# Performance work log

Hardware: AMD Instinct MI355X
Metric: run time of the kernel (lower is better)

Reference implementation:

```python
import jax, jax.numpy as jnp
import numpy as np

B, S, H = 256, 196, 1024  # batch, image_size**2, hidden_size


def _linear_init(key, fan_in, fan_out):
    kw, kb = jax.random.split(key)
    lim = 1.0 / np.sqrt(fan_in)
    W = jax.random.uniform(kw, (fan_in, fan_out), jnp.float32, -lim, lim)
    b = jax.random.uniform(kb, (fan_out,), jnp.float32, -lim, lim)
    return W, b


def setup_inputs() -> dict:
    key = jax.random.key(0)
    ks = jax.random.split(key, 7)
    v = jax.random.normal(ks[0], (B, S, H), jnp.float32)
    h = jax.random.normal(ks[1], (B, H), jnp.float32)
    W_fc, b_fc = _linear_init(ks[2], H, 2 * H)
    W_v, b_v = _linear_init(ks[3], H, H)
    W_h, b_h = _linear_init(ks[4], H, H)
    W_s, b_s = _linear_init(ks[5], H, H)
    W_z, b_z = _linear_init(ks[6], H, 1)
    return {"v": v, "h": h, "W_fc": W_fc, "b_fc": b_fc, "W_v": W_v, "b_v": b_v,
            "W_h": W_h, "b_h": b_h, "W_s": W_s, "b_s": b_s, "W_z": W_z, "b_z": b_z}


def reference(v, h, W_fc, b_fc, W_v, b_v, W_h, b_h, W_s, b_s, W_z, b_z):
    # Dropout is identity in eval mode.
    hs = jnp.tanh(h[:, None, :] @ W_fc + b_fc)          # (B, 1, 2H)
    h1, s = hs[..., :H], hs[..., H:]                    # each (B, 1, H)
    _v = v @ W_v + b_v                                  # (B, S, H)
    _h = h1 @ W_h + b_h                                 # (B, 1, H)
    _s = s @ W_s + b_s                                  # (B, 1, H)
    z = jnp.tanh(jnp.concatenate([_v, _s], axis=1) + _h)  # (B, S+1, H)
    z = (z @ W_z + b_z)[..., 0]                         # (B, S+1)
    a = jax.nn.softmax(z, axis=1)                       # (B, S+1)
    vc = jnp.concatenate([v, s], axis=1)                # (B, S+1, H)
    c = jnp.sum(a[:, :, None] * vc, axis=1)             # (B, H)
    return a, c
```

## Files before the change

### kernel.cpp

```cpp
#include <hip/hip_runtime.h>
#include <hip/hip_bf16.h>
#include <cstdint>
#include <cstddef>

#define Bb  256
#define Ss  196
#define Hh  1024
#define SP1 197
#define Mm  50176

typedef float  f32x4 __attribute__((ext_vector_type(4)));
typedef short  s16x8 __attribute__((ext_vector_type(8)));
typedef unsigned short u16;
typedef unsigned short u16x8 __attribute__((ext_vector_type(8)));

__device__ __forceinline__ u16 f2b(float f) {
  __hip_bfloat16 b = __float2bfloat16(f);
  u16 r; __builtin_memcpy(&r, &b, 2); return r;
}

__device__ __forceinline__ float ftanh(float x) {
  float ax = fabsf(x);
  float t = __expf(-2.f * ax);
  float r = (1.f - t) * __builtin_amdgcn_rcpf(1.f + t);
  return copysignf(r, x);
}

__global__ __launch_bounds__(256) void k_transpose_cvt(const float* __restrict__ Wv,
                                                       u16* __restrict__ WvT) {
  __shared__ float t[64][65];
  int k0 = (blockIdx.x & 15) * 64;
  int n0 = (blockIdx.x >> 4) * 64;
  int tid = threadIdx.x;
#pragma unroll
  for (int i = 0; i < 16; ++i) {
    int idx = i * 256 + tid;
    int r = idx >> 6, c = idx & 63;
    t[r][c] = Wv[(size_t)(k0 + r) * Hh + n0 + c];
  }
  __syncthreads();
#pragma unroll
  for (int i = 0; i < 16; ++i) {
    int idx = i * 256 + tid;
    int r = idx >> 6, c = idx & 63;
    WvT[(size_t)(n0 + r) * Hh + ((k0 + c) ^ ((r & 7) << 3))] = f2b(t[c][r]);
  }
}

__device__ __forceinline__ void small_gemm_core(int bid, int nct,
    const float* __restrict__ X, int ldx,
    const float* __restrict__ W, int ldw,
    const float* __restrict__ bias,
    float* __restrict__ Y, int ldy, int act) {
  __shared__ float xs[4][16][64];
  int tid = threadIdx.x, lane = tid & 63, w = tid >> 6;
  int ct = bid % nct, bt = bid / nct;
  int col = ct * 64 + lane;
  float acc[16];
#pragma unroll
  for (int b = 0; b < 16; ++b) acc[b] = 0.f;
  int xr = lane >> 2, xc = (lane & 3) * 16;
  for (int kc = 0; kc < 4; ++kc) {
    int kb = w * 256 + kc * 64;
#pragma unroll
    for (int q = 0; q < 4; ++q)
      *(f32x4*)&xs[w][xr][xc + q * 4] =
          *(const f32x4*)&X[(size_t)(bt * 16 + xr) * ldx + kb + xc + q * 4];
    for (int kl = 0; kl < 64; kl += 4) {
      float w0 = W[(size_t)(kb + kl + 0) * ldw + col];
      float w1 = W[(size_t)(kb + kl + 1) * ldw + col];
      float w2 = W[(size_t)(kb + kl + 2) * ldw + col];
      float w3 = W[(size_t)(kb + kl + 3) * ldw + col];
#pragma unroll
      for (int b = 0; b < 16; ++b) {
        f32x4 x = *(const f32x4*)&xs[w][b][kl];
        acc[b] += x.x * w0 + x.y * w1 + x.z * w2 + x.w * w3;
      }
    }
  }
#pragma unroll
  for (int b = 0; b < 16; ++b) xs[w][b][lane] = acc[b];
  __syncthreads();
#pragma unroll
  for (int q = 0; q < 4; ++q) {
    int b = w * 4 + q;
    float s = xs[0][b][lane] + xs[1][b][lane] + xs[2][b][lane] + xs[3][b][lane]
            + bias[col];
    if (act) s = ftanh(s);
    Y[(size_t)(bt * 16 + b) * ldy + col] = s;
  }
}

__global__ __launch_bounds__(256) void k_fc(const float* __restrict__ h,
                                            const float* __restrict__ Wfc,
                                            const float* __restrict__ bfc,
                                            float* __restrict__ hs) {
  small_gemm_core(blockIdx.x, 32, h, Hh, Wfc, 2048, bfc, hs, 2048, 1);
}

__global__ __launch_bounds__(256) void k_dual(const float* __restrict__ hs,
                                              const float* __restrict__ Wh,
                                              const float* __restrict__ bh,
                                              const float* __restrict__ Ws_,
                                              const float* __restrict__ bs_,
                                              float* __restrict__ hhp,
                                              float* __restrict__ svp) {
  int bid = blockIdx.x;
  int sel = bid >= 256;
  small_gemm_core(bid - (sel << 8), 16,
                  sel ? hs + 1024 : hs, 2048,
                  sel ? Ws_ : Wh, Hh,
                  sel ? bs_ : bh,
                  sel ? svp : hhp, Hh, 0);
}

#define BM 128
#define BN 256
#define BK 64
#define LDA 72
__global__ __launch_bounds__(256, 2) void k_big(const float* __restrict__ V,
                                                const u16* __restrict__ WvT,
                                                const float* __restrict__ bv,
                                                const float* __restrict__ hh,
                                                const float* __restrict__ Wz,
                                                float* __restrict__ zpart) {
  __shared__ __align__(16) u16 As[BM * LDA];
  __shared__ __align__(16) u16 Bs[BN * BK];
  __shared__ float wz_s[BN], bv_s[BN], hh_s[2][BN];
  __shared__ float zred[4][BM];

  int bid = blockIdx.x;
  int lin = (bid & 7) * 196 + (bid >> 3);
  int mt = lin >> 2, nt = lin & 3;
  int row0 = mt * BM, n0 = nt * BN;

  int tid = threadIdx.x;
  int lane = tid & 63, wid = tid >> 6;

  int b0 = row0 / Ss;
  int rsplit = (b0 + 1) * Ss - row0;
  int b1 = (rsplit < BM) ? b0 + 1 : b0;
  wz_s[tid] = Wz[n0 + tid];
  bv_s[tid] = bv[n0 + tid];
  hh_s[0][tid] = hh[(size_t)b0 * Hh + n0 + tid];
  hh_s[1][tid] = hh[(size_t)b1 * Hh + n0 + tid];

  f32x4 acc[8][4];
  f32x4 zz = {0.f, 0.f, 0.f, 0.f};
#pragma unroll
  for (int m = 0; m < 8; ++m)
#pragma unroll
    for (int n = 0; n < 4; ++n) acc[m][n] = zz;

  int arow = tid >> 3;
  int acol = (tid & 7) * 8;
  const float* Ap = V + (size_t)(row0 + arow) * Hh + acol;

  int bsub = lane >> 3;
  int bko  = (lane & 7) * 8;
  int bxor = (lane & 7) << 3;

  f32x4 av[8];
#pragma unroll
  for (int j = 0; j < 4; ++j) {
    av[2 * j]     = *(const f32x4*)(Ap + (size_t)j * 32 * Hh);
    av[2 * j + 1] = *(const f32x4*)(Ap + (size_t)j * 32 * Hh + 4);
  }

  for (int kt = 0; kt < 16; ++kt) {
    int k0 = kt * BK;
    __syncthreads();
#pragma unroll
    for (int i = 0; i < 8; ++i) {
      int r = wid * 64 + i * 8;
      const u16* g = WvT + (size_t)(n0 + r + bsub) * Hh + (k0 + bko);
      __builtin_amdgcn_global_load_lds(
          (const __attribute__((address_space(1))) unsigned int*)(const void*)g,
          (__attribute__((address_space(3))) unsigned int*)(void*)&Bs[r * BK],
          16, 0, 0);
    }
#pragma unroll
    for (int j = 0; j < 4; ++j) {
      u16x8 w;
      w[0] = f2b(av[2 * j].x);     w[1] = f2b(av[2 * j].y);
      w[2] = f2b(av[2 * j].z);     w[3] = f2b(av[2 * j].w);
      w[4] = f2b(av[2 * j + 1].x); w[5] = f2b(av[2 * j + 1].y);
      w[6] = f2b(av[2 * j + 1].z); w[7] = f2b(av[2 * j + 1].w);
      *(u16x8*)&As[(j * 32 + arow) * LDA + acol] = w;
    }
    if (kt < 15) {
#pragma unroll
      for (int j = 0; j < 4; ++j) {
        av[2 * j]     = *(const f32x4*)(Ap + (size_t)j * 32 * Hh + k0 + BK);
        av[2 * j + 1] = *(const f32x4*)(Ap + (size_t)j * 32 * Hh + k0 + BK + 4);
      }
    }
    __syncthreads();
#pragma unroll
    for (int ks = 0; ks < 2; ++ks) {
      int kk = ks * 32 + (lane >> 4) * 8;
      s16x8 afr[8], bfr[4];
#pragma unroll
      for (int m = 0; m < 8; ++m)
        afr[m] = *(const s16x8*)&As[(m * 16 + (lane & 15)) * LDA + kk];
#pragma unroll
      for (int n = 0; n < 4; ++n) {
        int r = wid * 64 + n * 16 + (lane & 15);
        bfr[n] = *(const s16x8*)&Bs[r * BK + (kk ^ bxor)];
      }
#pragma unroll
      for (int m = 0; m < 8; ++m)
#pragma unroll
        for (int n = 0; n < 4; ++n)
          acc[m][n] = __builtin_amdgcn_mfma_f32_16x16x32_bf16(afr[m], bfr[n], acc[m][n], 0, 0, 0);
    }
  }

  int cl = lane & 15, rg = lane >> 4;
  float pz[8][4];
#pragma unroll
  for (int m = 0; m < 8; ++m)
#pragma unroll
    for (int j = 0; j < 4; ++j) pz[m][j] = 0.f;
#pragma unroll
  for (int n = 0; n < 4; ++n) {
    int col = wid * 64 + n * 16 + cl;
    float wzv = wz_s[col], bvv = bv_s[col];
    float h0 = hh_s[0][col], h1 = hh_s[1][col];
#pragma unroll
    for (int m = 0; m < 8; ++m)
#pragma unroll
      for (int j = 0; j < 4; ++j) {
        int r = m * 16 + rg * 4 + j;
        float hv = (r >= rsplit) ? h1 : h0;
        pz[m][j] += wzv * ftanh(acc[m][n][j] + bvv + hv);
      }
  }
#pragma unroll
  for (int m = 0; m < 8; ++m)
#pragma unroll
    for (int j = 0; j < 4; ++j) {
      float vv = pz[m][j];
      vv += __shfl_xor(vv, 1); vv += __shfl_xor(vv, 2);
      vv += __shfl_xor(vv, 4); vv += __shfl_xor(vv, 8);
      pz[m][j] = vv;
    }
  if (cl == 0) {
#pragma unroll
    for (int m = 0; m < 8; ++m)
#pragma unroll
      for (int j = 0; j < 4; ++j)
        zred[wid][m * 16 + rg * 4 + j] = pz[m][j];
  }
  __syncthreads();
  if (tid < BM)
    zpart[(size_t)nt * Mm + row0 + tid] =
        zred[0][tid] + zred[1][tid] + zred[2][tid] + zred[3][tid];
}

__global__ __launch_bounds__(256) void k_softmax(const float* __restrict__ zpart,
                                                 const float* __restrict__ sv,
                                                 const float* __restrict__ hhp,
                                                 const float* __restrict__ Wz,
                                                 const float* __restrict__ bz,
                                                 float* __restrict__ outA) {
  int b = blockIdx.x, tid = threadIdx.x;
  int wid = tid >> 6, lane = tid & 63;
  __shared__ float redm[4], reds[4];
  __shared__ float zSsh;
  {
    int j0 = tid * 4;
    f32x4 s4 = *(const f32x4*)&sv[(size_t)b * Hh + j0];
    f32x4 h4 = *(const f32x4*)&hhp[(size_t)b * Hh + j0];
    f32x4 w4 = *(const f32x4*)&Wz[j0];
    float p = w4.x * ftanh(s4.x + h4.x) + w4.y * ftanh(s4.y + h4.y)
            + w4.z * ftanh(s4.z + h4.z) + w4.w * ftanh(s4.w + h4.w);
#pragma unroll
    for (int d = 1; d < 64; d <<= 1) p += __shfl_xor(p, d);
    if (lane == 0) redm[wid] = p;
    __syncthreads();
    if (tid == 0) zSsh = redm[0] + redm[1] + redm[2] + redm[3] + bz[0];
    __syncthreads();
  }
  float z = -1e30f;
  if (tid < Ss) {
    float s = 0.f;
#pragma unroll
    for (int nt = 0; nt < 4; ++nt) s += zpart[(size_t)nt * Mm + (size_t)b * Ss + tid];
    z = s + bz[0];
  } else if (tid == Ss) {
    z = zSsh;
  }
  float m = z;
#pragma unroll
  for (int d = 1; d < 64; d <<= 1) m = fmaxf(m, __shfl_xor(m, d));
  if (lane == 0) redm[wid] = m;
  __syncthreads();
  m = fmaxf(fmaxf(redm[0], redm[1]), fmaxf(redm[2], redm[3]));
  float e = (tid <= Ss) ? expf(z - m) : 0.f;
  float s = e;
#pragma unroll
  for (int d = 1; d < 64; d <<= 1) s += __shfl_xor(s, d);
  if (lane == 0) reds[wid] = s;
  __syncthreads();
  s = reds[0] + reds[1] + reds[2] + reds[3];
  if (tid <= Ss) outA[(size_t)b * SP1 + tid] = e / s;
}

__global__ __launch_bounds__(256) void k_ctx(const float* __restrict__ V,
                                             const float* __restrict__ hs,
                                             const float* __restrict__ A,
                                             float* __restrict__ outC) {
  int b = blockIdx.x >> 2;
  int col = (blockIdx.x & 3) * 256 + threadIdx.x;
  __shared__ float a_s[SP1];
  if (threadIdx.x < SP1) a_s[threadIdx.x] = A[(size_t)b * SP1 + threadIdx.x];
  __syncthreads();
  float acc = a_s[Ss] * hs[(size_t)b * 2048 + 1024 + col];
  const float* vb = &V[(size_t)b * Ss * Hh + col];
#pragma unroll 4
  for (int t = 0; t < Ss; ++t) acc += a_s[t] * vb[(size_t)t * Hh];
  outC[(size_t)b * Hh + col] = acc;
}

extern "C" void kernel_launch(void* const* d_in, const int* in_sizes, int n_in,
                              void* d_out, int out_size, void* d_ws, size_t ws_size,
                              hipStream_t stream) {
  const float* v   = (const float*)d_in[0];
  const float* h   = (const float*)d_in[1];
  const float* Wfc = (const float*)d_in[2];
  const float* bfc = (const float*)d_in[3];
  const float* Wv  = (const float*)d_in[4];
  const float* bv  = (const float*)d_in[5];
  const float* Wh  = (const float*)d_in[6];
  const float* bh  = (const float*)d_in[7];
  const float* Ws  = (const float*)d_in[8];
  const float* bs  = (const float*)d_in[9];
  const float* Wz  = (const float*)d_in[10];
  const float* bz  = (const float*)d_in[11];
  float* out  = (float*)d_out;
  float* outA = out;
  float* outC = out + (size_t)Bb * SP1;

  float* ws  = (float*)d_ws;
  float* hs  = ws;
  float* hh  = hs + 524288;
  float* sv  = hh + 262144;
  float* zp  = sv + 262144;
  u16*  WvT  = (u16*)(zp + 200704);

  k_transpose_cvt<<<256, 256, 0, stream>>>(Wv, WvT);
  k_fc<<<512, 256, 0, stream>>>(h, Wfc, bfc, hs);
  k_dual<<<512, 256, 0, stream>>>(hs, Wh, bh, Ws, bs, hh, sv);
  k_big<<<1568, 256, 0, stream>>>(v, WvT, bv, hh, Wz, zp);
  k_softmax<<<256, 256, 0, stream>>>(zp, sv, hh, Wz, bz, outA);
  k_ctx<<<1024, 256, 0, stream>>>(v, hs, outA, outC);
}
```

Before: 262.4 us.

## Pre-convert V to swizzled bf16, shrink GEMM tile, read bf16 V in context

Adds a pass that converts V to a swizzled bf16 copy in workspace. The main GEMM then streams A tiles straight to LDS through global_load_lds, and the tile shrinks from 128x256 to 128x128 on a 2x2 wave grid with higher occupancy. The context kernel reads the bf16 copy, halving its V traffic but applying bf16 rounding to V in the output c. The path only runs when the workspace is large enough, otherwise it falls back to fp32 V with the new tiling, and it adds an extra full read and write of V.

```diff
diff --git a/kernel.cpp b/kernel.cpp
--- a/kernel.cpp
+++ b/kernel.cpp
@@ -18,12 +18,19 @@
   __hip_bfloat16 b = __float2bfloat16(f);
   u16 r; __builtin_memcpy(&r, &b, 2); return r;
 }
-
+__device__ __forceinline__ float b2f(u16 u) {
+  return __uint_as_float(((unsigned)u) << 16);
+}
 __device__ __forceinline__ float ftanh(float x) {
   float ax = fabsf(x);
   float t = __expf(-2.f * ax);
   float r = (1.f - t) * __builtin_amdgcn_rcpf(1.f + t);
   return copysignf(r, x);
+}
+__device__ __forceinline__ void gload16(const u16* g, u16* l) {
+  __builtin_amdgcn_global_load_lds(
+      (const __attribute__((address_space(1))) unsigned int*)(const void*)g,
+      (__attribute__((address_space(3))) unsigned int*)(void*)l, 16, 0, 0);
 }
 
 __global__ __launch_bounds__(256) void k_transpose_cvt(const float* __restrict__ Wv,
@@ -45,6 +52,19 @@
     int r = idx >> 6, c = idx & 63;
     WvT[(size_t)(n0 + r) * Hh + ((k0 + c) ^ ((r & 7) << 3))] = f2b(t[c][r]);
   }
+}
+
+__global__ __launch_bounds__(256) void k_cvtV(const float* __restrict__ V,
+                                              u16* __restrict__ Vb) {
+  int c = blockIdx.x * 256 + threadIdx.x;
+  int m = c >> 7;
+  int k8 = (c & 127) << 3;
+  f32x4 a = *(const f32x4*)(V + (size_t)m * Hh + k8);
+  f32x4 b = *(const f32x4*)(V + (size_t)m * Hh + k8 + 4);
+  u16x8 w;
+  w[0] = f2b(a.x); w[1] = f2b(a.y); w[2] = f2b(a.z); w[3] = f2b(a.w);
+  w[4] = f2b(b.x); w[5] = f2b(b.y); w[6] = f2b(b.z); w[7] = f2b(b.w);
+  *(u16x8*)(Vb + (size_t)m * Hh + (k8 ^ ((m & 7) << 3))) = w;
 }
 
 __device__ __forceinline__ void small_gemm_core(int bid, int nct,
@@ -114,102 +134,108 @@
                   sel ? svp : hhp, Hh, 0);
 }
 
-#define BM 128
-#define BN 256
 #define BK 64
-#define LDA 72
-__global__ __launch_bounds__(256, 2) void k_big(const float* __restrict__ V,
-                                                const u16* __restrict__ WvT,
-                                                const float* __restrict__ bv,
-                                                const float* __restrict__ hh,
-                                                const float* __restrict__ Wz,
-                                                float* __restrict__ zpart) {
-  __shared__ __align__(16) u16 As[BM * LDA];
-  __shared__ __align__(16) u16 Bs[BN * BK];
-  __shared__ float wz_s[BN], bv_s[BN], hh_s[2][BN];
-  __shared__ float zred[4][BM];
+template<int PRE>
+__global__ __launch_bounds__(256, PRE ? 4 : 3)
+void k_big(const float* __restrict__ V, const u16* __restrict__ Vb,
+           const u16* __restrict__ WvT, const float* __restrict__ bv,
+           const float* __restrict__ hh, const float* __restrict__ Wz,
+           float* __restrict__ zpart) {
+  constexpr int LDA_ = PRE ? 64 : 72;
+  __shared__ __align__(16) u16 As[128 * LDA_];
+  __shared__ __align__(16) u16 Bs[128 * 64];
+  __shared__ float wz_s[128], bv_s[128], hh_s[2][128];
+  __shared__ float zred[4][64];
 
   int bid = blockIdx.x;
-  int lin = (bid & 7) * 196 + (bid >> 3);
-  int mt = lin >> 2, nt = lin & 3;
-  int row0 = mt * BM, n0 = nt * BN;
+  int lin = (bid & 7) * 392 + (bid >> 3);
+  int mt = lin >> 3, nt = lin & 7;
+  int row0 = mt * 128, n0 = nt * 128;
 
   int tid = threadIdx.x;
   int lane = tid & 63, wid = tid >> 6;
+  int wm = wid >> 1, wn = wid & 1;
 
   int b0 = row0 / Ss;
   int rsplit = (b0 + 1) * Ss - row0;
-  int b1 = (rsplit < BM) ? b0 + 1 : b0;
-  wz_s[tid] = Wz[n0 + tid];
-  bv_s[tid] = bv[n0 + tid];
-  hh_s[0][tid] = hh[(size_t)b0 * Hh + n0 + tid];
-  hh_s[1][tid] = hh[(size_t)b1 * Hh + n0 + tid];
-
-  f32x4 acc[8][4];
+  int b1 = (rsplit < 128) ? b0 + 1 : b0;
+  if (tid < 128) {
+    wz_s[tid] = Wz[n0 + tid];
+    bv_s[tid] = bv[n0 + tid];
+    hh_s[0][tid] = hh[(size_t)b0 * Hh + n0 + tid];
+    hh_s[1][tid] = hh[(size_t)b1 * Hh + n0 + tid];
+  }
+
+  f32x4 acc[4][4];
   f32x4 zz = {0.f, 0.f, 0.f, 0.f};
 #pragma unroll
-  for (int m = 0; m < 8; ++m)
+  for (int m = 0; m < 4; ++m)
 #pragma unroll
     for (int n = 0; n < 4; ++n) acc[m][n] = zz;
 
-  int arow = tid >> 3;
-  int acol = (tid & 7) * 8;
-  const float* Ap = V + (size_t)(row0 + arow) * Hh + acol;
-
-  int bsub = lane >> 3;
-  int bko  = (lane & 7) * 8;
+  int srow = lane >> 3, scol = (lane & 7) * 8;
   int bxor = (lane & 7) << 3;
 
+  int arow = tid >> 3, acol8 = (tid & 7) * 8;
+  const float* Ap = V + (size_t)(row0 + arow) * Hh + acol8;
   f32x4 av[8];
-#pragma unroll
-  for (int j = 0; j < 4; ++j) {
-    av[2 * j]     = *(const f32x4*)(Ap + (size_t)j * 32 * Hh);
-    av[2 * j + 1] = *(const f32x4*)(Ap + (size_t)j * 32 * Hh + 4);
+  if constexpr (!PRE) {
+#pragma unroll
+    for (int j = 0; j < 4; ++j) {
+      av[2 * j]     = *(const f32x4*)(Ap + (size_t)j * 32 * Hh);
+      av[2 * j + 1] = *(const f32x4*)(Ap + (size_t)j * 32 * Hh + 4);
+    }
   }
 
   for (int kt = 0; kt < 16; ++kt) {
     int k0 = kt * BK;
     __syncthreads();
 #pragma unroll
-    for (int i = 0; i < 8; ++i) {
-      int r = wid * 64 + i * 8;
-      const u16* g = WvT + (size_t)(n0 + r + bsub) * Hh + (k0 + bko);
-      __builtin_amdgcn_global_load_lds(
-          (const __attribute__((address_space(1))) unsigned int*)(const void*)g,
-          (__attribute__((address_space(3))) unsigned int*)(void*)&Bs[r * BK],
-          16, 0, 0);
-    }
-#pragma unroll
-    for (int j = 0; j < 4; ++j) {
-      u16x8 w;
-      w[0] = f2b(av[2 * j].x);     w[1] = f2b(av[2 * j].y);
-      w[2] = f2b(av[2 * j].z);     w[3] = f2b(av[2 * j].w);
-      w[4] = f2b(av[2 * j + 1].x); w[5] = f2b(av[2 * j + 1].y);
-      w[6] = f2b(av[2 * j + 1].z); w[7] = f2b(av[2 * j + 1].w);
-      *(u16x8*)&As[(j * 32 + arow) * LDA + acol] = w;
-    }
-    if (kt < 15) {
+    for (int i = 0; i < 4; ++i) {
+      int r = wid * 32 + i * 8;
+      gload16(WvT + (size_t)(n0 + r + srow) * Hh + k0 + scol, &Bs[r * 64]);
+    }
+    if constexpr (PRE) {
+#pragma unroll
+      for (int i = 0; i < 4; ++i) {
+        int r = wid * 32 + i * 8;
+        gload16(Vb + (size_t)(row0 + r + srow) * Hh + k0 + scol, &As[r * 64]);
+      }
+    } else {
 #pragma unroll
       for (int j = 0; j < 4; ++j) {
-        av[2 * j]     = *(const f32x4*)(Ap + (size_t)j * 32 * Hh + k0 + BK);
-        av[2 * j + 1] = *(const f32x4*)(Ap + (size_t)j * 32 * Hh + k0 + BK + 4);
+        u16x8 w;
+        w[0] = f2b(av[2 * j].x);     w[1] = f2b(av[2 * j].y);
+        w[2] = f2b(av[2 * j].z);     w[3] = f2b(av[2 * j].w);
+        w[4] = f2b(av[2 * j + 1].x); w[5] = f2b(av[2 * j + 1].y);
+        w[6] = f2b(av[2 * j + 1].z); w[7] = f2b(av[2 * j + 1].w);
+        *(u16x8*)&As[(j * 32 + arow) * LDA_ + acol8] = w;
+      }
+      if (kt < 15) {
+#pragma unroll
+        for (int j = 0; j < 4; ++j) {
+          av[2 * j]     = *(const f32x4*)(Ap + (size_t)j * 32 * Hh + k0 + BK);
+          av[2 * j + 1] = *(const f32x4*)(Ap + (size_t)j * 32 * Hh + k0 + BK + 4);
+        }
       }
     }
     __syncthreads();
 #pragma unroll
     for (int ks = 0; ks < 2; ++ks) {
       int kk = ks * 32 + (lane >> 4) * 8;
-      s16x8 afr[8], bfr[4];
-#pragma unroll
-      for (int m = 0; m < 8; ++m)
-        afr[m] = *(const s16x8*)&As[(m * 16 + (lane & 15)) * LDA + kk];
+      s16x8 afr[4], bfr[4];
+#pragma unroll
+      for (int m = 0; m < 4; ++m) {
+        int r = wm * 64 + m * 16 + (lane & 15);
+        afr[m] = *(const s16x8*)&As[r * LDA_ + (PRE ? (kk ^ bxor) : kk)];
+      }
 #pragma unroll
       for (int n = 0; n < 4; ++n) {
-        int r = wid * 64 + n * 16 + (lane & 15);
-        bfr[n] = *(const s16x8*)&Bs[r * BK + (kk ^ bxor)];
-      }
-#pragma unroll
-      for (int m = 0; m < 8; ++m)
+        int r = wn * 64 + n * 16 + (lane & 15);
+        bfr[n] = *(const s16x8*)&Bs[r * 64 + (kk ^ bxor)];
+      }
+#pragma unroll
+      for (int m = 0; m < 4; ++m)
 #pragma unroll
         for (int n = 0; n < 4; ++n)
           acc[m][n] = __builtin_amdgcn_mfma_f32_16x16x32_bf16(afr[m], bfr[n], acc[m][n], 0, 0, 0);
@@ -217,27 +243,27 @@
   }
 
   int cl = lane & 15, rg = lane >> 4;
-  float pz[8][4];
-#pragma unroll
-  for (int m = 0; m < 8; ++m)
+  float pz[4][4];
+#pragma unroll
+  for (int m = 0; m < 4; ++m)
 #pragma unroll
     for (int j = 0; j < 4; ++j) pz[m][j] = 0.f;
 #pragma unroll
   for (int n = 0; n < 4; ++n) {
-    int col = wid * 64 + n * 16 + cl;
+    int col = wn * 64 + n * 16 + cl;
     float wzv = wz_s[col], bvv = bv_s[col];
     float h0 = hh_s[0][col], h1 = hh_s[1][col];
 #pragma unroll
-    for (int m = 0; m < 8; ++m)
+    for (int m = 0; m < 4; ++m)
 #pragma unroll
       for (int j = 0; j < 4; ++j) {
-        int r = m * 16 + rg * 4 + j;
+        int r = wm * 64 + m * 16 + rg * 4 + j;
         float hv = (r >= rsplit) ? h1 : h0;
         pz[m][j] += wzv * ftanh(acc[m][n][j] + bvv + hv);
       }
   }
 #pragma unroll
-  for (int m = 0; m < 8; ++m)
+  for (int m = 0; m < 4; ++m)
 #pragma unroll
     for (int j = 0; j < 4; ++j) {
       float vv = pz[m][j];
@@ -247,15 +273,17 @@
     }
   if (cl == 0) {
 #pragma unroll
-    for (int m = 0; m < 8; ++m)
+    for (int m = 0; m < 4; ++m)
 #pragma unroll
       for (int j = 0; j < 4; ++j)
         zred[wid][m * 16 + rg * 4 + j] = pz[m][j];
   }
   __syncthreads();
-  if (tid < BM)
+  if (tid < 128) {
+    int hhalf = tid >> 6, lr = tid & 63;
     zpart[(size_t)nt * Mm + row0 + tid] =
-        zred[0][tid] + zred[1][tid] + zred[2][tid] + zred[3][tid];
+        zred[hhalf * 2][lr] + zred[hhalf * 2 + 1][lr];
+  }
 }
 
 __global__ __launch_bounds__(256) void k_softmax(const float* __restrict__ zpart,
@@ -286,7 +314,7 @@
   if (tid < Ss) {
     float s = 0.f;
 #pragma unroll
-    for (int nt = 0; nt < 4; ++nt) s += zpart[(size_t)nt * Mm + (size_t)b * Ss + tid];
+    for (int nt = 0; nt < 8; ++nt) s += zpart[(size_t)nt * Mm + (size_t)b * Ss + tid];
     z = s + bz[0];
   } else if (tid == Ss) {
     z = zSsh;
@@ -307,7 +335,9 @@
   if (tid <= Ss) outA[(size_t)b * SP1 + tid] = e / s;
 }
 
+template<int PRE>
 __global__ __launch_bounds__(256) void k_ctx(const float* __restrict__ V,
+                                             const u16* __restrict__ Vb,
                                              const float* __restrict__ hs,
                                              const float* __restrict__ A,
                                              float* __restrict__ outC) {
@@ -317,9 +347,18 @@
   if (threadIdx.x < SP1) a_s[threadIdx.x] = A[(size_t)b * SP1 + threadIdx.x];
   __syncthreads();
   float acc = a_s[Ss] * hs[(size_t)b * 2048 + 1024 + col];
-  const float* vb = &V[(size_t)b * Ss * Hh + col];
+  if constexpr (PRE) {
+    size_t m0 = (size_t)b * Ss;
 #pragma unroll 4
-  for (int t = 0; t < Ss; ++t) acc += a_s[t] * vb[(size_t)t * Hh];
+    for (int t = 0; t < Ss; ++t) {
+      size_t m = m0 + t;
+      acc += a_s[t] * b2f(Vb[m * Hh + (col ^ (((int)m & 7) << 3))]);
+    }
+  } else {
+    const float* vb = V + (size_t)b * Ss * Hh + col;
+#pragma unroll 4
+    for (int t = 0; t < Ss; ++t) acc += a_s[t] * vb[(size_t)t * Hh];
+  }
   outC[(size_t)b * Hh + col] = acc;
 }
 
@@ -347,12 +386,21 @@
   float* hh  = hs + 524288;
   float* sv  = hh + 262144;
   float* zp  = sv + 262144;
-  u16*  WvT  = (u16*)(zp + 200704);
+  u16*  WvT  = (u16*)(zp + 401408);
+  u16*  Vb   = (u16*)((char*)(void*)WvT + 2097152);
+
+  bool pre = ws_size >= 110657536ull;
 
   k_transpose_cvt<<<256, 256, 0, stream>>>(Wv, WvT);
   k_fc<<<512, 256, 0, stream>>>(h, Wfc, bfc, hs);
   k_dual<<<512, 256, 0, stream>>>(hs, Wh, bh, Ws, bs, hh, sv);
-  k_big<<<1568, 256, 0, stream>>>(v, WvT, bv, hh, Wz, zp);
+  if (pre) {
+    k_cvtV<<<25088, 256, 0, stream>>>(v, Vb);
+    k_big<1><<<3136, 256, 0, stream>>>(v, Vb, WvT, bv, hh, Wz, zp);
+  } else {
+    k_big<0><<<3136, 256, 0, stream>>>(v, Vb, WvT, bv, hh, Wz, zp);
+  }
   k_softmax<<<256, 256, 0, stream>>>(zp, sv, hh, Wz, bz, outA);
-  k_ctx<<<1024, 256, 0, stream>>>(v, hs, outA, outC);
-}
+  if (pre) k_ctx<1><<<1024, 256, 0, stream>>>(v, Vb, hs, outA, outC);
+  else     k_ctx<0><<<1024, 256, 0, stream>>>(v, Vb, hs, outA, outC);
+}
```

Result: slower. 300.4 us (+14.5%).
